# Optimization experiments

Measured on AMD Instinct MI355X. Metric: run time of the kernel, lower is better.

## Reference

```python
import jax, jax.numpy as jnp
import numpy as np
import math

N, D, BITS = 2048, 1024, 8
K = 1 << BITS          # 256 centroids
NG = (D + 1) // 2      # 512 rotation groups

def setup_inputs() -> dict:
    key = jax.random.key(0)
    kx, kc, kr = jax.random.split(key, 3)
    x = jax.random.normal(kx, (N, D), dtype=jnp.float32)
    # Lloyd-Max style scalar codebook: sorted centroids for a Gaussian source
    centroids = jnp.sort(jax.random.normal(kc, (K,), dtype=jnp.float32))
    # random planar rotations: [cos(theta), sin(theta)] per 2D group
    angles = jax.random.uniform(kr, (NG,), dtype=jnp.float32) * (2.0 * math.pi)
    rot2 = jnp.stack([jnp.cos(angles), jnp.sin(angles)], axis=-1)  # [NG, 2]
    return {"x": x, "centroids": centroids, "rot2": rot2}

def reference(x, centroids, rot2):
    d = x.shape[-1]
    n_groups = rot2.shape[0]
    d_padded = 2 * n_groups
    # unit-normalize rows
    norms = jnp.clip(jnp.linalg.norm(x, axis=-1, keepdims=True), 1e-8)  # [N,1]
    x_unit = x / norms
    pad = d_padded - d
    if pad > 0:
        x_unit = jnp.pad(x_unit, [(0, 0)] * (x.ndim - 1) + [(0, pad)])
    v = x_unit.reshape(*x.shape[:-1], n_groups, 2)                      # [N,NG,2]
    c, s = rot2[..., 0], rot2[..., 1]
    v0, v1 = v[..., 0], v[..., 1]
    v_rot = jnp.stack([c * v0 - s * v1, s * v0 + c * v1], axis=-1)      # rotate
    flat = v_rot.reshape(*v_rot.shape[:-2], -1)                         # [N,d_padded]
    # per-scalar nearest-centroid quantization
    indices = jnp.argmin(jnp.abs(flat[..., None] - centroids), axis=-1) # [N,d_padded]
    values = centroids[indices]
    v_q = values.reshape(*values.shape[:-1], n_groups, 2)
    q0, q1 = v_q[..., 0], v_q[..., 1]
    v_rec = jnp.stack([c * q0 + s * q1, -s * q0 + c * q1], axis=-1)     # inverse rotate
    x_hat = v_rec.reshape(*v_rec.shape[:-2], -1)[..., :d] * norms       # rescale
    return (x_hat, indices)
```

## Files before the change

### kernel.cpp

```cpp
#include <hip/hip_runtime.h>
#include <cfloat>

#define NROWS 2048
#define DDIM  1024
#define KCEN  256

__global__ __launch_bounds__(256)
void planar_quant_kernel(const float* __restrict__ x,
                         const float* __restrict__ cen,
                         const float* __restrict__ rot,
                         float* __restrict__ out_xhat,
                         float* __restrict__ out_idx)
{
    __shared__ float s_cen[KCEN];
    __shared__ float s_mid[KCEN];
    __shared__ float s_red[4];
    __shared__ float s_norm;

    const int row = blockIdx.x;
    const int t   = threadIdx.x;

    s_cen[t] = cen[t];
    __syncthreads();
    s_mid[t] = (t < KCEN - 1) ? 0.5f * (s_cen[t] + s_cen[t + 1]) : FLT_MAX;

    const float4 xv = *(const float4*)(x + (size_t)row * DDIM + 4 * t);
    const float4 rv = *(const float4*)(rot + 4 * t);

    float ss = xv.x * xv.x + xv.y * xv.y + xv.z * xv.z + xv.w * xv.w;
    #pragma unroll
    for (int off = 32; off >= 1; off >>= 1)
        ss += __shfl_xor(ss, off, 64);
    if ((t & 63) == 0) s_red[t >> 6] = ss;
    __syncthreads();
    if (t == 0) {
        float tot = s_red[0] + s_red[1] + s_red[2] + s_red[3];
        s_norm = fmaxf(sqrtf(tot), 1e-8f);
    }
    __syncthreads();
    const float nrm = s_norm;
    const float inv = 1.0f / nrm;

    float v0 = xv.x * inv, v1 = xv.y * inv, v2 = xv.z * inv, v3 = xv.w * inv;

    float r[4];
    r[0] = rv.x * v0 - rv.y * v1;
    r[1] = rv.y * v0 + rv.x * v1;
    r[2] = rv.z * v2 - rv.w * v3;
    r[3] = rv.w * v2 + rv.z * v3;

    int   qi[4];
    float qv[4];
    #pragma unroll
    for (int e = 0; e < 4; ++e) {
        const float v = r[e];
        int idx = 0;
        #pragma unroll
        for (int step = 128; step >= 1; step >>= 1) {
            if (s_mid[idx + step - 1] < v) idx += step;
        }
        float best = fabsf(v - s_cen[idx]);
        if (idx > 0 && fabsf(v - s_cen[idx - 1]) <= best) {
            idx -= 1;
        } else if (idx < KCEN - 1 && fabsf(v - s_cen[idx + 1]) < best) {
            idx += 1;
        }
        qi[e] = idx;
        qv[e] = s_cen[idx];
    }

    float4 xh;
    xh.x = ( rv.x * qv[0] + rv.y * qv[1]) * nrm;
    xh.y = (-rv.y * qv[0] + rv.x * qv[1]) * nrm;
    xh.z = ( rv.z * qv[2] + rv.w * qv[3]) * nrm;
    xh.w = (-rv.w * qv[2] + rv.z * qv[3]) * nrm;

    float4 fi;
    fi.x = (float)qi[0]; fi.y = (float)qi[1]; fi.z = (float)qi[2]; fi.w = (float)qi[3];

    const size_t off = (size_t)row * DDIM + 4 * t;
    *(float4*)(out_xhat + off) = xh;
    *(float4*)(out_idx  + off) = fi;
}

extern "C" void kernel_launch(void* const* d_in, const int* in_sizes, int n_in,
                              void* d_out, int out_size, void* d_ws, size_t ws_size,
                              hipStream_t stream) {
    const float* x   = (const float*)d_in[0];
    const float* cen = (const float*)d_in[1];
    const float* rot = (const float*)d_in[2];
    float* out       = (float*)d_out;

    planar_quant_kernel<<<NROWS, 256, 0, stream>>>(
        x, cen, rot, out, out + (size_t)NROWS * DDIM);
}
```

Before: 69.28 us.

## Replace per-element binary search with a precomputed bucket LUT and local walk

Adds a small prep kernel that builds a 2048-entry lookup table mapping uniform buckets over [-1,1] to a starting centroid index. The main kernel copies this table into shared memory and uses it to seed each search, then walks linearly to correct the index, instead of running an 8-step binary search over midpoints. This is meant to cut the dependent shared-memory loads in the quantization loop, at the cost of an extra launch, an 8KB shared-memory fill per block, and data-dependent while loops that may diverge across lanes.

```diff
diff --git a/kernel.cpp b/kernel.cpp
--- a/kernel.cpp
+++ b/kernel.cpp
@@ -1,19 +1,41 @@
 #include <hip/hip_runtime.h>
 #include <cfloat>
 
-#define NROWS 2048
-#define DDIM  1024
-#define KCEN  256
+#define NROWS    2048
+#define DDIM     1024
+#define KCEN     256
+#define LUT_SIZE 2048
+
+__global__ __launch_bounds__(256)
+void prep_lut_kernel(const float* __restrict__ cen, int* __restrict__ lut) {
+    __shared__ float s_cen[KCEN];
+    __shared__ float s_mid[KCEN];
+    const int t = threadIdx.x;
+    s_cen[t] = cen[t];
+    __syncthreads();
+    s_mid[t] = (t < KCEN - 1) ? 0.5f * (s_cen[t] + s_cen[t + 1]) : FLT_MAX;
+    __syncthreads();
+
+    const int e = blockIdx.x * 256 + t;
+    const float g = -1.0f + (float)e * (2.0f / LUT_SIZE);
+    int idx = 0;
+    #pragma unroll
+    for (int s = 128; s >= 1; s >>= 1)
+        if (s_mid[idx + s - 1] < g) idx += s;
+    lut[e] = idx;
+}
 
 __global__ __launch_bounds__(256)
 void planar_quant_kernel(const float* __restrict__ x,
                          const float* __restrict__ cen,
                          const float* __restrict__ rot,
+                         const int*   __restrict__ lut,
                          float* __restrict__ out_xhat,
                          float* __restrict__ out_idx)
 {
     __shared__ float s_cen[KCEN];
     __shared__ float s_mid[KCEN];
+    __shared__ int   s_lut[LUT_SIZE];
     __shared__ float s_red[4];
     __shared__ float s_norm;
 
@@ -21,6 +43,8 @@
     const int t   = threadIdx.x;
 
     s_cen[t] = cen[t];
+    ((int4*)s_lut)[t]       = ((const int4*)lut)[t];
+    ((int4*)s_lut)[256 + t] = ((const int4*)lut)[256 + t];
     __syncthreads();
     s_mid[t] = (t < KCEN - 1) ? 0.5f * (s_cen[t] + s_cen[t + 1]) : FLT_MAX;
 
@@ -42,7 +66,6 @@
     const float inv = 1.0f / nrm;
 
     float v0 = xv.x * inv, v1 = xv.y * inv, v2 = xv.z * inv, v3 = xv.w * inv;
-
     float r[4];
     r[0] = rv.x * v0 - rv.y * v1;
     r[1] = rv.y * v0 + rv.x * v1;
@@ -54,11 +77,11 @@
     #pragma unroll
     for (int e = 0; e < 4; ++e) {
         const float v = r[e];
-        int idx = 0;
-        #pragma unroll
-        for (int step = 128; step >= 1; step >>= 1) {
-            if (s_mid[idx + step - 1] < v) idx += step;
-        }
+        int j = (int)((v + 1.0f) * (LUT_SIZE * 0.5f));
+        j = min(max(j, 0), LUT_SIZE - 1);
+        int idx = s_lut[j];
+        while (idx > 0 && s_mid[idx - 1] >= v) --idx;
+        while (s_mid[idx] < v) ++idx;
         float best = fabsf(v - s_cen[idx]);
         if (idx > 0 && fabsf(v - s_cen[idx - 1]) <= best) {
             idx -= 1;
@@ -90,7 +113,9 @@
     const float* cen = (const float*)d_in[1];
     const float* rot = (const float*)d_in[2];
     float* out       = (float*)d_out;
+    int*   lut       = (int*)d_ws;
 
+    prep_lut_kernel<<<LUT_SIZE / 256, 256, 0, stream>>>(cen, lut);
     planar_quant_kernel<<<NROWS, 256, 0, stream>>>(
-        x, cen, rot, out, out + (size_t)NROWS * DDIM);
+        x, cen, rot, lut, out, out + (size_t)NROWS * DDIM);
 }
```

Measured after the change: 71.12 us. 2.7% more time.

## Map one wavefront per row to drop block-level norm reduction syncs

Applied to the files above, without the earlier changes.

Each 64-lane wavefront now owns a whole row, with four rows per 256-thread block, so the row norm is computed with a wave shuffle reduction alone. This removes the shared-memory cross-wave reduction and two block barriers, and amortizes the centroid and midpoint table setup over four rows. All loads are issued before the table setup to overlap memory latency. Each thread now holds 16 elements plus rotation values, which raises register pressure, and the grid shrinks to 512 blocks.

```diff
diff --git a/kernel.cpp b/kernel.cpp
--- a/kernel.cpp
+++ b/kernel.cpp
@@ -4,6 +4,7 @@
 #define NROWS 2048
 #define DDIM  1024
 #define KCEN  256
+#define ROWS_PER_BLOCK 4
 
 __global__ __launch_bounds__(256)
 void planar_quant_kernel(const float* __restrict__ x,
@@ -14,73 +15,84 @@
 {
     __shared__ float s_cen[KCEN];
     __shared__ float s_mid[KCEN];
-    __shared__ float s_red[4];
-    __shared__ float s_norm;
 
-    const int row = blockIdx.x;
-    const int t   = threadIdx.x;
+    const int t    = threadIdx.x;
+    const int wave = t >> 6;
+    const int lane = t & 63;
+    const int row  = blockIdx.x * ROWS_PER_BLOCK + wave;
+    const size_t base = (size_t)row * DDIM;
+
+    float4 xv[4], rv[4];
+    #pragma unroll
+    for (int k = 0; k < 4; ++k) {
+        const int c = lane + 64 * k;
+        xv[k] = *(const float4*)(x + base + 4 * c);
+        rv[k] = *(const float4*)(rot + 4 * c);
+    }
 
     s_cen[t] = cen[t];
     __syncthreads();
     s_mid[t] = (t < KCEN - 1) ? 0.5f * (s_cen[t] + s_cen[t + 1]) : FLT_MAX;
 
-    const float4 xv = *(const float4*)(x + (size_t)row * DDIM + 4 * t);
-    const float4 rv = *(const float4*)(rot + 4 * t);
-
-    float ss = xv.x * xv.x + xv.y * xv.y + xv.z * xv.z + xv.w * xv.w;
+    float ss = 0.0f;
+    #pragma unroll
+    for (int k = 0; k < 4; ++k)
+        ss += xv[k].x * xv[k].x + xv[k].y * xv[k].y
+            + xv[k].z * xv[k].z + xv[k].w * xv[k].w;
     #pragma unroll
     for (int off = 32; off >= 1; off >>= 1)
         ss += __shfl_xor(ss, off, 64);
-    if ((t & 63) == 0) s_red[t >> 6] = ss;
-    __syncthreads();
-    if (t == 0) {
-        float tot = s_red[0] + s_red[1] + s_red[2] + s_red[3];
-        s_norm = fmaxf(sqrtf(tot), 1e-8f);
-    }
-    __syncthreads();
-    const float nrm = s_norm;
+    const float nrm = fmaxf(sqrtf(ss), 1e-8f);
     const float inv = 1.0f / nrm;
 
-    float v0 = xv.x * inv, v1 = xv.y * inv, v2 = xv.z * inv, v3 = xv.w * inv;
+    __syncthreads();
 
-    float r[4];
-    r[0] = rv.x * v0 - rv.y * v1;
-    r[1] = rv.y * v0 + rv.x * v1;
-    r[2] = rv.z * v2 - rv.w * v3;
-    r[3] = rv.w * v2 + rv.z * v3;
+    #pragma unroll
+    for (int k = 0; k < 4; ++k) {
+        const int c = lane + 64 * k;
+        const float4 xc = xv[k];
+        const float4 rc = rv[k];
 
-    int   qi[4];
-    float qv[4];
-    #pragma unroll
-    for (int e = 0; e < 4; ++e) {
-        const float v = r[e];
-        int idx = 0;
+        const float v0 = xc.x * inv, v1 = xc.y * inv;
+        const float v2 = xc.z * inv, v3 = xc.w * inv;
+        float r[4];
+        r[0] = rc.x * v0 - rc.y * v1;
+        r[1] = rc.y * v0 + rc.x * v1;
+        r[2] = rc.z * v2 - rc.w * v3;
+        r[3] = rc.w * v2 + rc.z * v3;
+
+        int   qi[4];
+        float qv[4];
         #pragma unroll
-        for (int step = 128; step >= 1; step >>= 1) {
-            if (s_mid[idx + step - 1] < v) idx += step;
+        for (int e = 0; e < 4; ++e) {
+            const float v = r[e];
+            int idx = 0;
+            #pragma unroll
+            for (int step = 128; step >= 1; step >>= 1)
+                if (s_mid[idx + step - 1] < v) idx += step;
+            float best = fabsf(v - s_cen[idx]);
+            if (idx > 0 && fabsf(v - s_cen[idx - 1]) <= best) {
+                idx -= 1;
+            } else if (idx < KCEN - 1 && fabsf(v - s_cen[idx + 1]) < best) {
+                idx += 1;
+            }
+            qi[e] = idx;
+            qv[e] = s_cen[idx];
         }
-        float best = fabsf(v - s_cen[idx]);
-        if (idx > 0 && fabsf(v - s_cen[idx - 1]) <= best) {
-            idx -= 1;
-        } else if (idx < KCEN - 1 && fabsf(v - s_cen[idx + 1]) < best) {
-            idx += 1;
-        }
-        qi[e] = idx;
-        qv[e] = s_cen[idx];
+
+        float4 xh;
+        xh.x = ( rc.x * qv[0] + rc.y * qv[1]) * nrm;
+        xh.y = (-rc.y * qv[0] + rc.x * qv[1]) * nrm;
+        xh.z = ( rc.z * qv[2] + rc.w * qv[3]) * nrm;
+        xh.w = (-rc.w * qv[2] + rc.z * qv[3]) * nrm;
+
+        float4 fi;
+        fi.x = (float)qi[0]; fi.y = (float)qi[1];
+        fi.z = (float)qi[2]; fi.w = (float)qi[3];
+
+        *(float4*)(out_xhat + base + 4 * c) = xh;
+        *(float4*)(out_idx  + base + 4 * c) = fi;
     }
-
-    float4 xh;
-    xh.x = ( rv.x * qv[0] + rv.y * qv[1]) * nrm;
-    xh.y = (-rv.y * qv[0] + rv.x * qv[1]) * nrm;
-    xh.z = ( rv.z * qv[2] + rv.w * qv[3]) * nrm;
-    xh.w = (-rv.w * qv[2] + rv.z * qv[3]) * nrm;
-
-    float4 fi;
-    fi.x = (float)qi[0]; fi.y = (float)qi[1]; fi.z = (float)qi[2]; fi.w = (float)qi[3];
-
-    const size_t off = (size_t)row * DDIM + 4 * t;
-    *(float4*)(out_xhat + off) = xh;
-    *(float4*)(out_idx  + off) = fi;
 }
 
 extern "C" void kernel_launch(void* const* d_in, const int* in_sizes, int n_in,
@@ -91,6 +103,6 @@
     const float* rot = (const float*)d_in[2];
     float* out       = (float*)d_out;
 
-    planar_quant_kernel<<<NROWS, 256, 0, stream>>>(
+    planar_quant_kernel<<<NROWS / ROWS_PER_BLOCK, 256, 0, stream>>>(
         x, cen, rot, out, out + (size_t)NROWS * DDIM);
 }
```

New measurement: 72.94 us. 1.05x slower.
